# Kernel optimization log

Measured on AMD Instinct MI355X. Metric: run time of the kernel, lower is better.

## Reference

```python
import jax, jax.numpy as jnp
import numpy as np

B, S, D = 2, 2048, 2048
H, DH = 16, 128


def _rope(x, position):
    # x: [B, H, S, DH], position: [B, S]
    dh = x.shape[-1]
    inv_freq = 1.0 / (10000.0 ** (jnp.arange(0, dh, 2, dtype=jnp.float32) / dh))
    freqs = position.astype(jnp.float32)[:, :, None] * inv_freq[None, None, :]  # [B, S, DH/2]
    emb = jnp.concatenate([freqs, freqs], axis=-1)  # [B, S, DH]
    cos = jnp.cos(emb)[:, None, :, :]
    sin = jnp.sin(emb)[:, None, :, :]
    x1, x2 = x[..., : dh // 2], x[..., dh // 2 :]
    rot = jnp.concatenate([-x2, x1], axis=-1)
    return x * cos + rot * sin


def setup_inputs() -> dict:
    key = jax.random.key(0)
    ks = jax.random.split(key, 5)
    hidden_state = jax.random.normal(ks[0], (B, S, D), dtype=jnp.float32)
    mask = jnp.broadcast_to(jnp.tril(jnp.ones((S, S), dtype=bool)), (B, S, S))
    position = jnp.broadcast_to(jnp.arange(S, dtype=jnp.int64), (B, S))
    scale = 1.0 / np.sqrt(D)
    Wq = jax.random.normal(ks[1], (D, H * DH), dtype=jnp.float32) * scale
    Wk = jax.random.normal(ks[2], (D, H * DH), dtype=jnp.float32) * scale
    Wv = jax.random.normal(ks[3], (D, H * DH), dtype=jnp.float32) * scale
    Wo = jax.random.normal(ks[4], (H * DH, D), dtype=jnp.float32) * scale
    return {"hidden_state": hidden_state, "mask": mask, "position": position,
            "Wq": Wq, "Wk": Wk, "Wv": Wv, "Wo": Wo}


def reference(hidden_state, mask, position, Wq, Wk, Wv, Wo):
    b, s, _ = hidden_state.shape
    def split_heads(h):
        return h.reshape(b, s, H, DH).transpose(0, 2, 1, 3)  # [B, H, S, DH]
    h_q = _rope(split_heads(hidden_state @ Wq), position)
    h_k = _rope(split_heads(hidden_state @ Wk), position)
    h_v = split_heads(hidden_state @ Wv)
    score = jnp.einsum('bhqd,bhkd->bhqk', h_q, h_k) / np.sqrt(DH)
    m = mask[:, None, :, :]
    score = jnp.where(m, score, jnp.float32(-jnp.inf))
    probs = jax.nn.softmax(score, axis=-1)
    probs = jnp.where(m, probs, jnp.float32(0.0))
    out = jnp.einsum('bhqk,bhkd->bhqd', probs, h_v)
    out = out.transpose(0, 2, 1, 3).reshape(b, s, H * DH)
    return out @ Wo
```

## Files before the change

### kernel.cpp

```cpp
#include <hip/hip_runtime.h>
#include <hip/hip_bf16.h>

typedef unsigned short u16;
typedef __bf16 bf16x8 __attribute__((ext_vector_type(8)));
typedef float f32x4 __attribute__((ext_vector_type(4)));
typedef unsigned short u16x8 __attribute__((ext_vector_type(8)));
typedef unsigned short u16x4 __attribute__((ext_vector_type(4)));

__device__ __forceinline__ u16 f2bf(float f) {
  union { float f; unsigned u; } v; v.f = f;
  unsigned r = (v.u + 0x7FFFu + ((v.u >> 16) & 1u)) >> 16;
  return (u16)r;
}
__device__ __forceinline__ float bf2f(u16 s) {
  union { unsigned u; float f; } v; v.u = ((unsigned)s) << 16;
  return v.f;
}
__device__ __forceinline__ f32x4 zero4() { f32x4 z = {0.f, 0.f, 0.f, 0.f}; return z; }

__device__ __forceinline__ void async16(void* lds, const void* g) {
  __builtin_amdgcn_global_load_lds(
      (__attribute__((address_space(1))) void*)(void*)g,
      (__attribute__((address_space(3))) void*)lds, 16, 0, 0);
}

__global__ void sniff_dtype(const unsigned* __restrict__ X, int* __restrict__ flag) {
  __shared__ int cnt;
  if (threadIdx.x == 0) cnt = 0;
  __syncthreads();
  unsigned w = X[(size_t)threadIdx.x * 16384 + 1000];
  int e = (int)((w >> 7) & 0xFF);
  if (e >= 100 && e <= 150) atomicAdd(&cnt, 1);
  __syncthreads();
  if (threadIdx.x == 0) flag[0] = (cnt < 192) ? 1 : 0;
}

__global__ __launch_bounds__(256) void convert_x(
    const void* __restrict__ X, u16* __restrict__ dst, const int* __restrict__ flag) {
  const int mode = flag[0];
  size_t i8 = ((size_t)blockIdx.x * 256 + threadIdx.x) * 8;
  if (mode) {
    const float4* f = (const float4*)X;
    float4 a = f[i8 / 4], b = f[i8 / 4 + 1];
    u16x8 o;
    o[0] = f2bf(a.x); o[1] = f2bf(a.y); o[2] = f2bf(a.z); o[3] = f2bf(a.w);
    o[4] = f2bf(b.x); o[5] = f2bf(b.y); o[6] = f2bf(b.z); o[7] = f2bf(b.w);
    *(u16x8*)&dst[i8] = o;
  } else {
    *(u16x8*)&dst[i8] = *(const u16x8*)&((const u16*)X)[i8];
  }
}

__global__ __launch_bounds__(256) void convert_out(
    const float* __restrict__ src, void* __restrict__ dst, const int* __restrict__ flag) {
  const int mode = flag[0];
  size_t i4 = ((size_t)blockIdx.x * 256 + threadIdx.x) * 4;
  float4 v = *(const float4*)&src[i4];
  if (mode) {
    *(float4*)&((float*)dst)[i4] = v;
  } else {
    u16x4 o;
    o[0] = f2bf(v.x); o[1] = f2bf(v.y); o[2] = f2bf(v.z); o[3] = f2bf(v.w);
    *(u16x4*)&((u16*)dst)[i4] = o;
  }
}

__global__ __launch_bounds__(256) void transpose_w(
    const void* __restrict__ src, u16* __restrict__ d, const int* __restrict__ flag)
{
  __shared__ u16 t[64][65];
  const int mode = flag[0];
  int r0 = blockIdx.y * 64, c0 = blockIdx.x * 64;
  int tid = threadIdx.x;
  for (int j = 0; j < 2; ++j) {
    int idx = tid + j * 256;
    int r = idx >> 3, c = (idx & 7) * 8;
    size_t base = (size_t)(r0 + r) * 2048 + c0 + c;
    if (mode) {
      const float4* f = (const float4*)src;
      float4 a = f[base / 4], b = f[base / 4 + 1];
      t[r][c + 0] = f2bf(a.x); t[r][c + 1] = f2bf(a.y);
      t[r][c + 2] = f2bf(a.z); t[r][c + 3] = f2bf(a.w);
      t[r][c + 4] = f2bf(b.x); t[r][c + 5] = f2bf(b.y);
      t[r][c + 6] = f2bf(b.z); t[r][c + 7] = f2bf(b.w);
    } else {
      u16x8 v = *(const u16x8*)&((const u16*)src)[base];
      for (int q = 0; q < 8; ++q) t[r][c + q] = v[q];
    }
  }
  __syncthreads();
  for (int j = 0; j < 2; ++j) {
    int idx = tid + j * 256;
    int c = idx >> 3, r = (idx & 7) * 8;
    u16x8 v;
    for (int q = 0; q < 8; ++q) v[q] = t[r + q][c];
    *(u16x8*)&d[(size_t)(c0 + c) * 2048 + r0 + r] = v;
  }
}

__global__ __launch_bounds__(256) void transpose_v(
    const u16* __restrict__ V, u16* __restrict__ Vt)
{
  __shared__ u16 t[64][65];
  int bh = blockIdx.z;
  int b = bh >> 4, h = bh & 15;
  int kv0 = blockIdx.x * 64, d0 = blockIdx.y * 64;
  int tid = threadIdx.x;
  for (int j = 0; j < 2; ++j) {
    int idx = tid + j * 256;
    int r = idx >> 3, c = (idx & 7) * 8;
    u16x8 v = *(const u16x8*)&V[(size_t)(b * 2048 + kv0 + r) * 2048 + h * 128 + d0 + c];
    for (int q = 0; q < 8; ++q) t[r][c + q] = v[q];
  }
  __syncthreads();
  for (int j = 0; j < 2; ++j) {
    int idx = tid + j * 256;
    int c = idx >> 3, r = (idx & 7) * 8;
    u16x8 v;
    for (int q = 0; q < 8; ++q) v[q] = t[r + q][c];
    *(u16x8*)&Vt[((size_t)bh * 128 + d0 + c) * 2048 + kv0 + r] = v;
  }
}

__global__ __launch_bounds__(256) void rope_k(u16* __restrict__ Qp, u16* __restrict__ Kp)
{
  int idx = blockIdx.x * 256 + threadIdx.x;
  u16* X = blockIdx.y ? Kp : Qp;
  int i8 = (idx & 7) * 8;
  int hq = (idx >> 3) & 3;
  int tok = idx >> 5;
  int pos = tok & 2047;

  float c8[8], s8[8];
  for (int j = 0; j < 8; ++j) {
    float fi = (float)(i8 + j);
    float invf = __expf(fi * -0.14391156831212787f);
    float th = (float)pos * invf;
    sincosf(th, &s8[j], &c8[j]);
  }

  for (int hh = 0; hh < 4; ++hh) {
    int h = hq * 4 + hh;
    size_t base = (size_t)tok * 2048 + h * 128 + i8;
    u16x8 a = *(const u16x8*)&X[base];
    u16x8 bv = *(const u16x8*)&X[base + 64];
    u16x8 ra, rb;
    for (int j = 0; j < 8; ++j) {
      float x1 = bf2f(a[j]), x2 = bf2f(bv[j]);
      ra[j] = f2bf(x1 * c8[j] - x2 * s8[j]);
      rb[j] = f2bf(x2 * c8[j] + x1 * s8[j]);
    }
    *(u16x8*)&X[base] = ra;
    *(u16x8*)&X[base + 64] = rb;
  }
}

__device__ __forceinline__ void qkv_compute(
    const u16* As, const u16* Bs, f32x4 (&acc)[4][4],
    int wr, int wc, int quad, int l)
{
  bf16x8 af[4], bfr[4];
  for (int mt = 0; mt < 4; ++mt) {
    int row = wr * 64 + mt * 16 + l;
    int g = quad ^ ((row >> 1) & 3);
    af[mt] = *(const bf16x8*)&As[row * 32 + g * 8];
  }
  for (int nt = 0; nt < 4; ++nt) {
    int row = wc * 64 + nt * 16 + l;
    int g = quad ^ ((row >> 1) & 3);
    bfr[nt] = *(const bf16x8*)&Bs[row * 32 + g * 8];
  }
  for (int mt = 0; mt < 4; ++mt)
    for (int nt = 0; nt < 4; ++nt)
      acc[mt][nt] = __builtin_amdgcn_mfma_f32_16x16x32_bf16(af[mt], bfr[nt], acc[mt][nt], 0, 0, 0);
}

__global__ __launch_bounds__(256) void qkv_gemm(
    const u16* __restrict__ A, const u16* __restrict__ Bt,
    u16* __restrict__ Qw, u16* __restrict__ Kw, u16* __restrict__ Vw)
{
  __shared__ __align__(16) u16 As0[128 * 32];
  __shared__ __align__(16) u16 Bs0[128 * 32];
  __shared__ __align__(16) u16 As1[128 * 32];
  __shared__ __align__(16) u16 Bs1[128 * 32];
  const int K = 2048, N = 2048;
  const int tid = threadIdx.x;
  const int wave = tid >> 6, lane = tid & 63;
  const int quad = lane >> 4, l = lane & 15;
  const int wr = wave >> 1, wc = wave & 1;
  const int m0 = blockIdx.y * 128, n0full = blockIdx.x * 128;
  const int mat = n0full >> 11;
  const int n0 = n0full & 2047;
  u16* C = (mat == 0) ? Qw : ((mat == 1) ? Kw : Vw);

  f32x4 acc[4][4];
  for (int i = 0; i < 4; ++i)
    for (int j = 0; j < 4; ++j) acc[i][j] = zero4();

  const int rowA0 = tid >> 2;
  const int gA0 = (tid & 3) ^ ((rowA0 >> 1) & 3);
  const int rowA1 = (tid + 256) >> 2;
  const int gA1 = ((tid + 256) & 3) ^ ((rowA1 >> 1) & 3);

  const u16* pA0 = &A[(size_t)(m0 + rowA0) * 2048 + gA0 * 8];
  const u16* pA1 = &A[(size_t)(m0 + rowA1) * 2048 + gA1 * 8];
  const u16* pB0 = &Bt[(size_t)(n0full + rowA0) * 2048 + gA0 * 8];
  const u16* pB1 = &Bt[(size_t)(n0full + rowA1) * 2048 + gA1 * 8];

  u16* dA0s0 = &As0[tid * 8];        u16* dA1s0 = &As0[(tid + 256) * 8];
  u16* dB0s0 = &Bs0[tid * 8];        u16* dB1s0 = &Bs0[(tid + 256) * 8];
  u16* dA0s1 = &As1[tid * 8];        u16* dA1s1 = &As1[(tid + 256) * 8];
  u16* dB0s1 = &Bs1[tid * 8];        u16* dB1s1 = &Bs1[(tid + 256) * 8];

  async16(dA0s0, pA0); async16(dA1s0, pA1);
  async16(dB0s0, pB0); async16(dB1s0, pB1);
  __syncthreads();

  for (int kt = 0; kt < K; kt += 64) {
    async16(dA0s1, pA0 + 32); async16(dA1s1, pA1 + 32);
    async16(dB0s1, pB0 + 32); async16(dB1s1, pB1 + 32);
    qkv_compute(As0, Bs0, acc, wr, wc, quad, l);
    __syncthreads();
    if (kt + 64 < K) {
      async16(dA0s0, pA0 + 64); async16(dA1s0, pA1 + 64);
      async16(dB0s0, pB0 + 64); async16(dB1s0, pB1 + 64);
    }
    qkv_compute(As1, Bs1, acc, wr, wc, quad, l);
    __syncthreads();
    pA0 += 64; pA1 += 64; pB0 += 64; pB1 += 64;
  }

  for (int mt = 0; mt < 4; ++mt)
    for (int nt = 0; nt < 4; ++nt)
      for (int r = 0; r < 4; ++r) {
        int m = m0 + wr * 64 + mt * 16 + quad * 4 + r;
        int n = n0 + wc * 64 + nt * 16 + l;
        C[(size_t)m * N + n] = f2bf(acc[mt][nt][r]);
      }
}

__global__ __launch_bounds__(256) void gemm128_wo(
    const u16* __restrict__ A, const u16* __restrict__ Bt, float* __restrict__ Wf)
{
  __shared__ __align__(16) u16 As0[128 * 32];
  __shared__ __align__(16) u16 Bs0[128 * 32];
  __shared__ __align__(16) u16 As1[128 * 32];
  __shared__ __align__(16) u16 Bs1[128 * 32];
  const int K = 2048, N = 2048;
  const int tid = threadIdx.x;
  const int wave = tid >> 6, lane = tid & 63;
  const int quad = lane >> 4, l = lane & 15;
  const int wr = wave >> 1, wc = wave & 1;
  const int m0 = blockIdx.y * 128, n0 = blockIdx.x * 128;

  f32x4 acc[4][4];
  for (int i = 0; i < 4; ++i)
    for (int j = 0; j < 4; ++j) acc[i][j] = zero4();

  const int rowA0 = tid >> 2;
  const int gA0 = (tid & 3) ^ ((rowA0 >> 1) & 3);
  const int rowA1 = (tid + 256) >> 2;
  const int gA1 = ((tid + 256) & 3) ^ ((rowA1 >> 1) & 3);

  const u16* pA0 = &A[(size_t)(m0 + rowA0) * 2048 + gA0 * 8];
  const u16* pA1 = &A[(size_t)(m0 + rowA1) * 2048 + gA1 * 8];
  const u16* pB0 = &Bt[(size_t)(n0 + rowA0) * 2048 + gA0 * 8];
  const u16* pB1 = &Bt[(size_t)(n0 + rowA1) * 2048 + gA1 * 8];

  u16* dA0s0 = &As0[tid * 8];        u16* dA1s0 = &As0[(tid + 256) * 8];
  u16* dB0s0 = &Bs0[tid * 8];        u16* dB1s0 = &Bs0[(tid + 256) * 8];
  u16* dA0s1 = &As1[tid * 8];        u16* dA1s1 = &As1[(tid + 256) * 8];
  u16* dB0s1 = &Bs1[tid * 8];        u16* dB1s1 = &Bs1[(tid + 256) * 8];

  async16(dA0s0, pA0); async16(dA1s0, pA1);
  async16(dB0s0, pB0); async16(dB1s0, pB1);
  __syncthreads();

  for (int kt = 0; kt < K; kt += 64) {
    async16(dA0s1, pA0 + 32); async16(dA1s1, pA1 + 32);
    async16(dB0s1, pB0 + 32); async16(dB1s1, pB1 + 32);
    qkv_compute(As0, Bs0, acc, wr, wc, quad, l);
    __syncthreads();
    if (kt + 64 < K) {
      async16(dA0s0, pA0 + 64); async16(dA1s0, pA1 + 64);
      async16(dB0s0, pB0 + 64); async16(dB1s0, pB1 + 64);
    }
    qkv_compute(As1, Bs1, acc, wr, wc, quad, l);
    __syncthreads();
    pA0 += 64; pA1 += 64; pB0 += 64; pB1 += 64;
  }

  for (int mt = 0; mt < 4; ++mt)
    for (int nt = 0; nt < 4; ++nt)
      for (int r = 0; r < 4; ++r) {
        int m = m0 + wr * 64 + mt * 16 + quad * 4 + r;
        int n = n0 + wc * 64 + nt * 16 + l;
        Wf[(size_t)m * N + n] = acc[mt][nt][r];
      }
}

__device__ __forceinline__ void fl_stage(
    u16* Ks, u16* Vs, const u16* K, const u16* Vt,
    size_t kbase, size_t vbase, int kt, int tid)
{
  for (int j = 0; j < 4; ++j) {
    int tf = tid + j * 256;
    int row = tf >> 4, p = tf & 15;
    int g = p ^ (row & 7);
    async16(&Ks[tf * 8], &K[kbase + (size_t)(kt * 64 + row) * 2048 + g * 8]);
  }
  for (int j = 0; j < 4; ++j) {
    int tf = tid + j * 256;
    int row = tf >> 3, p = tf & 7;
    int g = p ^ (row & 7);
    async16(&Vs[tf * 8], &Vt[vbase + (size_t)row * 2048 + kt * 64 + g * 8]);
  }
}

__global__ __launch_bounds__(256) void flash_k(
    const u16* __restrict__ Q, const u16* __restrict__ K,
    const u16* __restrict__ Vt, u16* __restrict__ O)
{
  __shared__ __align__(16) u16 Ks0[64 * 128];
  __shared__ __align__(16) u16 Vs0[128 * 64];
  __shared__ __align__(16) u16 Ks1[64 * 128];
  __shared__ __align__(16) u16 Vs1[128 * 64];
  __shared__ __align__(16) u16 Ps[4][16 * 64];

  const int tid = threadIdx.x;
  const int wave = tid >> 6, lane = tid & 63;
  const int quad = lane >> 4, l = lane & 15;
  const int pair = blockIdx.x;
  const int h = blockIdx.y, b = blockIdx.z;

  const size_t kbase = ((size_t)b * 2048) * 2048 + h * 128;
  const size_t vbase = ((size_t)(b * 16 + h)) * 128 * 2048;

  for (int half = 0; half < 2; ++half) {
    const int qt = half ? pair : (31 - pair);

    const size_t qoff = ((size_t)(b * 2048 + qt * 64)) * 2048 + h * 128;
    bf16x8 qf[4];
    for (int ks = 0; ks < 4; ++ks)
      qf[ks] = *(const bf16x8*)&Q[qoff + (size_t)(wave * 16 + l) * 2048 + (ks * 4 + quad) * 8];

    f32x4 Oacc[8];
    for (int i = 0; i < 8; ++i) Oacc[i] = zero4();
    float mi[4] = {-3e38f, -3e38f, -3e38f, -3e38f};
    float li[4] = {0.f, 0.f, 0.f, 0.f};

    auto fl_body = [&](const u16* Ksb, const u16* Vsb, int kt) {
      f32x4 S[4];
      for (int nt = 0; nt < 4; ++nt) S[nt] = zero4();
      for (int ks = 0; ks < 4; ++ks) {
        int g = ks * 4 + quad;
        for (int nt = 0; nt < 4; ++nt) {
          bf16x8 bk = *(const bf16x8*)&Ksb[(nt * 16 + l) * 128 + (g ^ (l & 7)) * 8];
          S[nt] = __builtin_amdgcn_mfma_f32_16x16x32_bf16(qf[ks], bk, S[nt], 0, 0, 0);
        }
      }

      const bool dg = (kt == qt);
      float Pv[4][4];
      float rm[4] = {-3e38f, -3e38f, -3e38f, -3e38f};
      for (int nt = 0; nt < 4; ++nt)
        for (int r = 0; r < 4; ++r) {
          float s = S[nt][r] * 0.08838834764831845f;
          if (dg && (nt * 16 + l > wave * 16 + quad * 4 + r)) s = -3e38f;
          Pv[nt][r] = s;
          rm[r] = fmaxf(rm[r], s);
        }
      for (int r = 0; r < 4; ++r)
        for (int off = 1; off < 16; off <<= 1)
          rm[r] = fmaxf(rm[r], __shfl_xor(rm[r], off));
      float al[4], rs[4];
      for (int r = 0; r < 4; ++r) {
        float mn = fmaxf(mi[r], rm[r]);
        al[r] = __expf(mi[r] - mn);
        mi[r] = mn;
        rs[r] = 0.f;
      }
      for (int nt = 0; nt < 4; ++nt)
        for (int r = 0; r < 4; ++r) {
          float p = __expf(Pv[nt][r] - mi[r]);
          Pv[nt][r] = p;
          rs[r] += p;
        }
      for (int r = 0; r < 4; ++r) {
        for (int off = 1; off < 16; off <<= 1)
          rs[r] += __shfl_xor(rs[r], off);
        li[r] = li[r] * al[r] + rs[r];
      }
      for (int nt = 0; nt < 4; ++nt) {
        int gc = nt * 2 + (l >> 3);
        for (int r = 0; r < 4; ++r) {
          int row = quad * 4 + r;
          Ps[wave][row * 64 + ((gc ^ (row & 7)) * 8) + (l & 7)] = f2bf(Pv[nt][r]);
        }
      }
      for (int d = 0; d < 8; ++d)
        for (int r = 0; r < 4; ++r) Oacc[d][r] *= al[r];
      for (int ks = 0; ks < 2; ++ks) {
        int g = ks * 4 + quad;
        bf16x8 ap = *(const bf16x8*)&Ps[wave][l * 64 + (g ^ (l & 7)) * 8];
        for (int d = 0; d < 8; ++d) {
          bf16x8 bv = *(const bf16x8*)&Vsb[(d * 16 + l) * 64 + (g ^ (l & 7)) * 8];
          Oacc[d] = __builtin_amdgcn_mfma_f32_16x16x32_bf16(ap, bv, Oacc[d], 0, 0, 0);
        }
      }
    };

    fl_stage(Ks0, Vs0, K, Vt, kbase, vbase, 0, tid);
    __syncthreads();

    for (int kt = 0; kt <= qt; kt += 2) {
      if (kt + 1 <= qt) fl_stage(Ks1, Vs1, K, Vt, kbase, vbase, kt + 1, tid);
      fl_body(Ks0, Vs0, kt);
      __syncthreads();
      if (kt + 1 <= qt) {
        if (kt + 2 <= qt) fl_stage(Ks0, Vs0, K, Vt, kbase, vbase, kt + 2, tid);
        fl_body(Ks1, Vs1, kt + 1);
        __syncthreads();
      }
    }

    float inv[4];
    for (int r = 0; r < 4; ++r) inv[r] = 1.f / li[r];
    size_t obase = ((size_t)(b * 2048 + qt * 64 + wave * 16)) * 2048 + h * 128;
    for (int d = 0; d < 8; ++d)
      for (int r = 0; r < 4; ++r)
        O[obase + (size_t)(quad * 4 + r) * 2048 + d * 16 + l] = f2bf(Oacc[d][r] * inv[r]);
  }
}

extern "C" void kernel_launch(void* const* d_in, const int* in_sizes, int n_in,
                              void* d_out, int out_size, void* d_ws, size_t ws_size,
                              hipStream_t stream) {
  const void* X  = d_in[0];
  const void* Wq = d_in[3];
  const void* Wk = d_in[4];
  const void* Wv = d_in[5];
  const void* Wo = d_in[6];

  u16* base = (u16*)d_ws;
  int* flag = (int*)d_ws;
  const size_t TOK = 4096, DM = 2048;
  u16* Xbf = base + 128;
  u16* Qw  = Xbf + TOK * DM;
  u16* Kw  = Qw + TOK * DM;
  u16* Vw  = Kw + TOK * DM;
  u16* WT3 = Vw + TOK * DM;
  u16* Vtw = Xbf;
  float* Wf = (float*)Xbf;

  sniff_dtype<<<1, 256, 0, stream>>>((const unsigned*)X, flag);
  convert_x<<<4096, 256, 0, stream>>>(X, Xbf, flag);

  transpose_w<<<dim3(32, 32), 256, 0, stream>>>(Wq, WT3, flag);
  transpose_w<<<dim3(32, 32), 256, 0, stream>>>(Wk, WT3 + DM * DM, flag);
  transpose_w<<<dim3(32, 32), 256, 0, stream>>>(Wv, WT3 + 2 * DM * DM, flag);
  qkv_gemm<<<dim3(48, 32), 256, 0, stream>>>(Xbf, WT3, Qw, Kw, Vw);

  rope_k<<<dim3(512, 2), 256, 0, stream>>>(Qw, Kw);
  transpose_v<<<dim3(32, 2, 32), 256, 0, stream>>>(Vw, Vtw);
  flash_k<<<dim3(16, 16, 2), 256, 0, stream>>>(Qw, Kw, Vtw, Vw);

  transpose_w<<<dim3(32, 32), 256, 0, stream>>>(Wo, WT3, flag);
  gemm128_wo<<<dim3(16, 32), 256, 0, stream>>>(Vw, WT3, Wf);
  convert_out<<<8192, 256, 0, stream>>>(Wf, d_out, flag);
}
```

Measured before the change: 460.4 us.

## Deepen GEMM K-loop pipeline to four LDS stages with vmcnt-gated barriers

Both the QKV and Wo GEMMs move from a double-buffered LDS pipeline to a four-stage ring, keeping three K-slices in flight. Each full __syncthreads is replaced by an explicit s_waitcnt vmcnt(N) plus s_barrier, so a wave waits only for the oldest slice rather than draining all outstanding loads. The aim is to hide global-load latency behind MFMA work. The cost is double the LDS per block, which may lower occupancy, and the hand-written waitcnt/barrier sequencing has to match the exact load count.

Measured after the change: 445.5 us. 1.03x faster.

```diff
diff --git a/kernel.cpp b/kernel.cpp
--- a/kernel.cpp
+++ b/kernel.cpp
@@ -23,6 +23,8 @@
       (__attribute__((address_space(1))) void*)(void*)g,
       (__attribute__((address_space(3))) void*)lds, 16, 0, 0);
 }
+
+#define WBAR(N) asm volatile("s_waitcnt vmcnt(" #N ")\n\ts_barrier" ::: "memory")
 
 __global__ void sniff_dtype(const unsigned* __restrict__ X, int* __restrict__ flag) {
   __shared__ int cnt;
@@ -179,11 +181,11 @@
     const u16* __restrict__ A, const u16* __restrict__ Bt,
     u16* __restrict__ Qw, u16* __restrict__ Kw, u16* __restrict__ Vw)
 {
-  __shared__ __align__(16) u16 As0[128 * 32];
-  __shared__ __align__(16) u16 Bs0[128 * 32];
-  __shared__ __align__(16) u16 As1[128 * 32];
-  __shared__ __align__(16) u16 Bs1[128 * 32];
-  const int K = 2048, N = 2048;
+  __shared__ __align__(16) u16 As0[128 * 32], Bs0[128 * 32];
+  __shared__ __align__(16) u16 As1[128 * 32], Bs1[128 * 32];
+  __shared__ __align__(16) u16 As2[128 * 32], Bs2[128 * 32];
+  __shared__ __align__(16) u16 As3[128 * 32], Bs3[128 * 32];
+  const int N = 2048;
   const int tid = threadIdx.x;
   const int wave = tid >> 6, lane = tid & 63;
   const int quad = lane >> 4, l = lane & 15;
@@ -207,28 +209,26 @@
   const u16* pB0 = &Bt[(size_t)(n0full + rowA0) * 2048 + gA0 * 8];
   const u16* pB1 = &Bt[(size_t)(n0full + rowA1) * 2048 + gA1 * 8];
 
-  u16* dA0s0 = &As0[tid * 8];        u16* dA1s0 = &As0[(tid + 256) * 8];
-  u16* dB0s0 = &Bs0[tid * 8];        u16* dB1s0 = &Bs0[(tid + 256) * 8];
-  u16* dA0s1 = &As1[tid * 8];        u16* dA1s1 = &As1[(tid + 256) * 8];
-  u16* dB0s1 = &Bs1[tid * 8];        u16* dB1s1 = &Bs1[(tid + 256) * 8];
-
-  async16(dA0s0, pA0); async16(dA1s0, pA1);
-  async16(dB0s0, pB0); async16(dB1s0, pB1);
-  __syncthreads();
-
-  for (int kt = 0; kt < K; kt += 64) {
-    async16(dA0s1, pA0 + 32); async16(dA1s1, pA1 + 32);
-    async16(dB0s1, pB0 + 32); async16(dB1s1, pB1 + 32);
-    qkv_compute(As0, Bs0, acc, wr, wc, quad, l);
-    __syncthreads();
-    if (kt + 64 < K) {
-      async16(dA0s0, pA0 + 64); async16(dA1s0, pA1 + 64);
-      async16(dB0s0, pB0 + 64); async16(dB1s0, pB1 + 64);
-    }
-    qkv_compute(As1, Bs1, acc, wr, wc, quad, l);
-    __syncthreads();
-    pA0 += 64; pA1 += 64; pB0 += 64; pB1 += 64;
-  }
+#define STG(AS, BS, OFF) \
+  async16(&AS[tid * 8], pA0 + (OFF)); async16(&AS[(tid + 256) * 8], pA1 + (OFF)); \
+  async16(&BS[tid * 8], pB0 + (OFF)); async16(&BS[(tid + 256) * 8], pB1 + (OFF));
+
+  STG(As0, Bs0, 0)
+  STG(As1, Bs1, 32)
+  STG(As2, Bs2, 64)
+
+  for (int g = 0; g < 15; ++g) {
+    WBAR(8); STG(As3, Bs3, 96)  qkv_compute(As0, Bs0, acc, wr, wc, quad, l);
+    WBAR(8); STG(As0, Bs0, 128) qkv_compute(As1, Bs1, acc, wr, wc, quad, l);
+    WBAR(8); STG(As1, Bs1, 160) qkv_compute(As2, Bs2, acc, wr, wc, quad, l);
+    WBAR(8); STG(As2, Bs2, 192) qkv_compute(As3, Bs3, acc, wr, wc, quad, l);
+    pA0 += 128; pA1 += 128; pB0 += 128; pB1 += 128;
+  }
+  WBAR(8); STG(As3, Bs3, 96)  qkv_compute(As0, Bs0, acc, wr, wc, quad, l);
+  WBAR(8); qkv_compute(As1, Bs1, acc, wr, wc, quad, l);
+  WBAR(4); qkv_compute(As2, Bs2, acc, wr, wc, quad, l);
+  WBAR(0); qkv_compute(As3, Bs3, acc, wr, wc, quad, l);
+#undef STG
 
   for (int mt = 0; mt < 4; ++mt)
     for (int nt = 0; nt < 4; ++nt)
@@ -242,11 +242,11 @@
 __global__ __launch_bounds__(256) void gemm128_wo(
     const u16* __restrict__ A, const u16* __restrict__ Bt, float* __restrict__ Wf)
 {
-  __shared__ __align__(16) u16 As0[128 * 32];
-  __shared__ __align__(16) u16 Bs0[128 * 32];
-  __shared__ __align__(16) u16 As1[128 * 32];
-  __shared__ __align__(16) u16 Bs1[128 * 32];
-  const int K = 2048, N = 2048;
+  __shared__ __align__(16) u16 As0[128 * 32], Bs0[128 * 32];
+  __shared__ __align__(16) u16 As1[128 * 32], Bs1[128 * 32];
+  __shared__ __align__(16) u16 As2[128 * 32], Bs2[128 * 32];
+  __shared__ __align__(16) u16 As3[128 * 32], Bs3[128 * 32];
+  const int N = 2048;
   const int tid = threadIdx.x;
   const int wave = tid >> 6, lane = tid & 63;
   const int quad = lane >> 4, l = lane & 15;
@@ -267,28 +267,26 @@
   const u16* pB0 = &Bt[(size_t)(n0 + rowA0) * 2048 + gA0 * 8];
   const u16* pB1 = &Bt[(size_t)(n0 + rowA1) * 2048 + gA1 * 8];
 
-  u16* dA0s0 = &As0[tid * 8];        u16* dA1s0 = &As0[(tid + 256) * 8];
-  u16* dB0s0 = &Bs0[tid * 8];        u16* dB1s0 = &Bs0[(tid + 256) * 8];
-  u16* dA0s1 = &As1[tid * 8];        u16* dA1s1 = &As1[(tid + 256) * 8];
-  u16* dB0s1 = &Bs1[tid * 8];        u16* dB1s1 = &Bs1[(tid + 256) * 8];
-
-  async16(dA0s0, pA0); async16(dA1s0, pA1);
-  async16(dB0s0, pB0); async16(dB1s0, pB1);
-  __syncthreads();
-
-  for (int kt = 0; kt < K; kt += 64) {
-    async16(dA0s1, pA0 + 32); async16(dA1s1, pA1 + 32);
-    async16(dB0s1, pB0 + 32); async16(dB1s1, pB1 + 32);
-    qkv_compute(As0, Bs0, acc, wr, wc, quad, l);
-    __syncthreads();
-    if (kt + 64 < K) {
-      async16(dA0s0, pA0 + 64); async16(dA1s0, pA1 + 64);
-      async16(dB0s0, pB0 + 64); async16(dB1s0, pB1 + 64);
-    }
-    qkv_compute(As1, Bs1, acc, wr, wc, quad, l);
-    __syncthreads();
-    pA0 += 64; pA1 += 64; pB0 += 64; pB1 += 64;
-  }
+#define STG(AS, BS, OFF) \
+  async16(&AS[tid * 8], pA0 + (OFF)); async16(&AS[(tid + 256) * 8], pA1 + (OFF)); \
+  async16(&BS[tid * 8], pB0 + (OFF)); async16(&BS[(tid + 256) * 8], pB1 + (OFF));
+
+  STG(As0, Bs0, 0)
+  STG(As1, Bs1, 32)
+  STG(As2, Bs2, 64)
+
+  for (int g = 0; g < 15; ++g) {
+    WBAR(8); STG(As3, Bs3, 96)  qkv_compute(As0, Bs0, acc, wr, wc, quad, l);
+    WBAR(8); STG(As0, Bs0, 128) qkv_compute(As1, Bs1, acc, wr, wc, quad, l);
+    WBAR(8); STG(As1, Bs1, 160) qkv_compute(As2, Bs2, acc, wr, wc, quad, l);
+    WBAR(8); STG(As2, Bs2, 192) qkv_compute(As3, Bs3, acc, wr, wc, quad, l);
+    pA0 += 128; pA1 += 128; pB0 += 128; pB1 += 128;
+  }
+  WBAR(8); STG(As3, Bs3, 96)  qkv_compute(As0, Bs0, acc, wr, wc, quad, l);
+  WBAR(8); qkv_compute(As1, Bs1, acc, wr, wc, quad, l);
+  WBAR(4); qkv_compute(As2, Bs2, acc, wr, wc, quad, l);
+  WBAR(0); qkv_compute(As3, Bs3, acc, wr, wc, quad, l);
+#undef STG
 
   for (int mt = 0; mt < 4; ++mt)
     for (int nt = 0; nt < 4; ++nt)
```
